# Kernel optimization log

Measured on AMD Instinct MI355X. Metric: run time of the kernel, lower is better.

## Reference

```python
import jax, jax.numpy as jnp
import numpy as np

OUT = 7  # out_size


def setup_inputs() -> dict:
    key = jax.random.key(0)
    kx, k1, k2, k3, k4 = jax.random.split(key, 5)
    B, C, H, W, Q = 4, 256, 128, 128, 100
    x = jax.random.normal(kx, (B, C, H, W), dtype=jnp.float32)
    # valid boxes: start in [0, W/2), extent in [8, W/2) -> always in-bounds, nonempty
    x1 = jax.random.randint(k1, (B, Q), 0, W // 2)
    y1 = jax.random.randint(k2, (B, Q), 0, H // 2)
    x2 = x1 + jax.random.randint(k3, (B, Q), 8, W // 2)
    y2 = y1 + jax.random.randint(k4, (B, Q), 8, H // 2)
    bidx = jnp.broadcast_to(jnp.arange(B, dtype=jnp.int32)[:, None], (B, Q))
    rois = jnp.stack([bidx, x1, y1, x2, y2], axis=-1).astype(jnp.int32)
    return {"x": x, "rois": rois}


def _bin_edges(start, length, nbins):
    # adaptive_avg_pool2d bin boundaries for bin k over a region of given length:
    #   lo_k = floor(k*L/n), hi_k = ceil((k+1)*L/n)
    # start, length: [B,Q] int; returns (starts, ends) each [B,Q,nbins]
    k = jnp.arange(nbins)
    lo = start[..., None] + (k * length[..., None]) // nbins
    hi = start[..., None] - ((-(k + 1) * length[..., None]) // nbins)  # ceil div
    return lo, hi


def reference(x, rois):
    # x: [B,C,H,W] float, rois: [B,Q,5] int (batch_idx, x1, y1, x2, y2)
    B, C, H, W = x.shape
    Q = rois.shape[1]
    oh = ow = OUT
    # Summed-area table S[b, y, x, c] = sum of x over rows < y, cols < x.
    xc = jnp.moveaxis(x, 1, -1)                       # [B,H,W,C]
    S = jnp.cumsum(jnp.cumsum(xc, axis=1), axis=2)
    S = jnp.pad(S, ((0, 0), (1, 0), (1, 0), (0, 0)))  # [B,H+1,W+1,C]

    x1, y1, x2, y2 = rois[..., 1], rois[..., 2], rois[..., 3], rois[..., 4]
    ys, ye = _bin_edges(y1, y2 - y1, oh)              # [B,Q,oh]
    xs, xe = _bin_edges(x1, x2 - x1, ow)              # [B,Q,ow]

    b = jnp.arange(B)[:, None, None, None]            # [B,1,1,1]
    Ys, Ye = ys[:, :, :, None], ye[:, :, :, None]     # [B,Q,oh,1]
    Xs, Xe = xs[:, :, None, :], xe[:, :, None, :]     # [B,Q,1,ow]

    # rectangle sums per bin via SAT corner differences -> [B,Q,oh,ow,C]
    sums = S[b, Ye, Xe] - S[b, Ys, Xe] - S[b, Ye, Xs] + S[b, Ys, Xs]
    area = ((Ye - Ys) * (Xe - Xs)).astype(x.dtype)[..., None]
    out = sums / area                                  # bin averages

    out = jnp.moveaxis(out, -1, 2)                     # [B,Q,C,oh,ow]
    return out.reshape(B, Q * C, oh, ow)               # cat ROIs along channel dim
```

## Files before the change

kernel.cpp:

```cpp
#include <hip/hip_runtime.h>

#define B_ 4
#define C_ 256
#define H_ 128
#define W_ 128
#define Q_ 100
#define WP_ 132

__global__ __launch_bounds__(512, 4) void roipool_kernel(const float4* __restrict__ x4,
                                                         const int* __restrict__ rois,
                                                         float* __restrict__ out) {
    __shared__ __align__(16) float sat[H_ * WP_];
    __shared__ float4 ot4[16 * 33];
    __shared__ unsigned int ebl[Q_ * 7];

    const int c   = blockIdx.x & 255;
    const int b   = blockIdx.x >> 8;
    const int tid = threadIdx.x;

    const float4* src = x4 + (size_t)(b * C_ + c) * (H_ * W_ / 4);
    const int wv = tid >> 6, ln = tid & 63;
    const int xl = ln & 31;
    #pragma unroll
    for (int i = 0; i < 8; ++i) {
        const int r = wv * 16 + i * 2 + (ln >> 5);
        float4 v = src[wv * 512 + i * 64 + ln];
        float s = v.x + v.y + v.z + v.w;
        float run = s;
        #pragma unroll
        for (int d = 1; d < 32; d <<= 1) {
            float t = __shfl_up(run, d);
            if (xl >= d) run += t;
        }
        const float excl = run - s;
        float4 o;
        o.x = excl + v.x;
        o.y = o.x + v.y;
        o.z = o.y + v.z;
        o.w = o.z + v.w;
        ((float4*)(sat + r * WP_))[xl] = o;
    }

    const int* rbase = rois + (size_t)b * Q_ * 5;
    for (int t = tid; t < Q_ * 7; t += 512) {
        const int q = t / 7;
        const int k = t - q * 7;
        const int* rb = rbase + q * 5;
        const int x1 = rb[1], y1 = rb[2];
        const int Lx = rb[3] - x1, Ly = rb[4] - y1;
        const unsigned int ys = y1 + (k * Ly) / 7;
        const unsigned int ye = y1 + ((k + 1) * Ly + 6) / 7;
        const unsigned int xs = x1 + (k * Lx) / 7;
        const unsigned int xe = x1 + ((k + 1) * Lx + 6) / 7;
        ebl[t] = ys | (ye << 8) | (xs << 16) | (xe << 24);
    }
    __syncthreads();

    {
        float4* s4 = (float4*)sat;
        const int oct = tid >> 5;
        const int stp = tid & 31;
        float4 acc = make_float4(0.f, 0.f, 0.f, 0.f);
        #pragma unroll
        for (int j = 0; j < 8; ++j) {
            const int y = oct * 8 + j;
            float4 v = s4[y * 33 + stp];
            acc.x += v.x; acc.y += v.y; acc.z += v.z; acc.w += v.w;
            s4[y * 33 + stp] = acc;
        }
        ot4[oct * 33 + stp] = acc;
    }
    __syncthreads();

    if (tid < 32) {
        float4 run = make_float4(0.f, 0.f, 0.f, 0.f);
        #pragma unroll
        for (int k = 0; k < 16; ++k) {
            float4 v = ot4[k * 33 + tid];
            ot4[k * 33 + tid] = run;
            run.x += v.x; run.y += v.y; run.z += v.z; run.w += v.w;
        }
    }
    __syncthreads();

    {
        float4* s4 = (float4*)sat;
        #pragma unroll
        for (int j = 0; j < 8; ++j) {
            const int f = j * 512 + tid;
            const int y = f >> 5;
            const int oc = y >> 3;
            const int st = f & 31;
            if (oc > 0) {
                float4 off = ot4[oc * 33 + st];
                float4 v = s4[y * 33 + st];
                v.x += off.x; v.y += off.y; v.z += off.z; v.w += off.w;
                s4[y * 33 + st] = v;
            }
        }
    }
    __syncthreads();

    float* ob = out + (size_t)(b * Q_) * (C_ * 49) + (size_t)c * 49;
    for (int t = tid; t < Q_ * 49; t += 512) {
        const int q   = t / 49;
        const int bin = t - q * 49;
        const int oy  = bin / 7;
        const int ox  = bin - oy * 7;

        const unsigned int ey = ebl[q * 7 + oy];
        const unsigned int ex = ebl[q * 7 + ox];
        const int ys = ey & 255;
        const int ye = (ey >> 8) & 255;
        const int xs = (ex >> 16) & 255;
        const int xe = ex >> 24;

        const float s11 = sat[(ye - 1) * WP_ + (xe - 1)];
        const float s01 = (ys > 0) ? sat[(ys - 1) * WP_ + (xe - 1)] : 0.f;
        const float s10 = (xs > 0) ? sat[(ye - 1) * WP_ + (xs - 1)] : 0.f;
        const float s00 = (ys > 0 && xs > 0) ? sat[(ys - 1) * WP_ + (xs - 1)] : 0.f;

        const float inv = __builtin_amdgcn_rcpf((float)((ye - ys) * (xe - xs)));
        ob[(size_t)q * (C_ * 49) + bin] = (s11 - s01 - s10 + s00) * inv;
    }
}

extern "C" void kernel_launch(void* const* d_in, const int* in_sizes, int n_in,
                              void* d_out, int out_size, void* d_ws, size_t ws_size,
                              hipStream_t stream) {
    const float* x    = (const float*)d_in[0];
    const int*   rois = (const int*)d_in[1];
    float*       outp = (float*)d_out;

    roipool_kernel<<<B_ * C_, 512, 0, stream>>>((const float4*)x, rois, outp);
}
```

Before: 108.1 us.

## Reorder SAT build: column scan from registers, then DPP row scan with padding

The summed-area table build is restructured. Global loads now feed the column prefix directly in registers instead of first scanning rows and writing to LDS. The row scan is fused with the column-offset fixup pass and uses DPP row-shift instructions in place of shfl_up. The table gains a zero row and a zero column at offset 3, so the query loop can drop its boundary branches. Together these remove one LDS read/write pass, the shuffle overhead and a barrier, at the cost of relying on wave-specific DPP semantics that must span a 32-lane half correctly.

```diff
diff --git a/kernel.cpp b/kernel.cpp
--- a/kernel.cpp
+++ b/kernel.cpp
@@ -5,12 +5,28 @@
 #define H_ 128
 #define W_ 128
 #define Q_ 100
-#define WP_ 132
+#define WROW 132
+#define NROW 129
+
+__device__ __forceinline__ float dpp_scan32(float s) {
+    int t;
+    t = __builtin_amdgcn_update_dpp(0, __float_as_int(s), 0x111, 0xf, 0xf, true);
+    s += __int_as_float(t);
+    t = __builtin_amdgcn_update_dpp(0, __float_as_int(s), 0x112, 0xf, 0xf, true);
+    s += __int_as_float(t);
+    t = __builtin_amdgcn_update_dpp(0, __float_as_int(s), 0x114, 0xf, 0xf, true);
+    s += __int_as_float(t);
+    t = __builtin_amdgcn_update_dpp(0, __float_as_int(s), 0x118, 0xf, 0xf, true);
+    s += __int_as_float(t);
+    t = __builtin_amdgcn_update_dpp(0, __float_as_int(s), 0x142, 0xa, 0xf, true);
+    s += __int_as_float(t);
+    return s;
+}
 
 __global__ __launch_bounds__(512, 4) void roipool_kernel(const float4* __restrict__ x4,
                                                          const int* __restrict__ rois,
                                                          float* __restrict__ out) {
-    __shared__ __align__(16) float sat[H_ * WP_];
+    __shared__ __align__(16) float sat[NROW * WROW];
     __shared__ float4 ot4[16 * 33];
     __shared__ unsigned int ebl[Q_ * 7];
 
@@ -18,30 +34,10 @@
     const int b   = blockIdx.x >> 8;
     const int tid = threadIdx.x;
 
-    const float4* src = x4 + (size_t)(b * C_ + c) * (H_ * W_ / 4);
-    const int wv = tid >> 6, ln = tid & 63;
-    const int xl = ln & 31;
-    #pragma unroll
-    for (int i = 0; i < 8; ++i) {
-        const int r = wv * 16 + i * 2 + (ln >> 5);
-        float4 v = src[wv * 512 + i * 64 + ln];
-        float s = v.x + v.y + v.z + v.w;
-        float run = s;
-        #pragma unroll
-        for (int d = 1; d < 32; d <<= 1) {
-            float t = __shfl_up(run, d);
-            if (xl >= d) run += t;
-        }
-        const float excl = run - s;
-        float4 o;
-        o.x = excl + v.x;
-        o.y = o.x + v.y;
-        o.z = o.y + v.z;
-        o.w = o.z + v.w;
-        ((float4*)(sat + r * WP_))[xl] = o;
-    }
+    if (tid < WROW) sat[tid] = 0.f;
+    else if (tid < WROW + 128) sat[(tid - WROW + 1) * WROW + 3] = 0.f;
 
-    const int* rbase = rois + (size_t)b * Q_ * 5;
+    const int* rbase = rois + b * Q_ * 5;
     for (int t = tid; t < Q_ * 7; t += 512) {
         const int q = t / 7;
         const int k = t - q * 7;
@@ -50,23 +46,24 @@
         const int Lx = rb[3] - x1, Ly = rb[4] - y1;
         const unsigned int ys = y1 + (k * Ly) / 7;
         const unsigned int ye = y1 + ((k + 1) * Ly + 6) / 7;
-        const unsigned int xs = x1 + (k * Lx) / 7;
-        const unsigned int xe = x1 + ((k + 1) * Lx + 6) / 7;
+        const unsigned int xs = x1 + (k * Lx) / 7 + 3;
+        const unsigned int xe = x1 + ((k + 1) * Lx + 6) / 7 + 3;
         ebl[t] = ys | (ye << 8) | (xs << 16) | (xe << 24);
     }
-    __syncthreads();
 
     {
-        float4* s4 = (float4*)sat;
         const int oct = tid >> 5;
         const int stp = tid & 31;
-        float4 acc = make_float4(0.f, 0.f, 0.f, 0.f);
+        const float4* src = x4 + (size_t)(b * C_ + c) * (H_ * W_ / 4);
+        float4 v[8];
+        #pragma unroll
+        for (int j = 0; j < 8; ++j)
+            v[j] = src[(oct * 8 + j) * 32 + stp];
+        float4 acc = v[0];
         #pragma unroll
         for (int j = 0; j < 8; ++j) {
-            const int y = oct * 8 + j;
-            float4 v = s4[y * 33 + stp];
-            acc.x += v.x; acc.y += v.y; acc.z += v.z; acc.w += v.w;
-            s4[y * 33 + stp] = acc;
+            if (j) { acc.x += v[j].x; acc.y += v[j].y; acc.z += v[j].z; acc.w += v[j].w; }
+            ((float4*)(sat + (oct * 8 + j + 1) * WROW + 4))[stp] = acc;
         }
         ot4[oct * 33 + stp] = acc;
     }
@@ -84,19 +81,24 @@
     __syncthreads();
 
     {
-        float4* s4 = (float4*)sat;
+        const int wv = tid >> 6, ln = tid & 63;
+        const int xl = ln & 31;
         #pragma unroll
-        for (int j = 0; j < 8; ++j) {
-            const int f = j * 512 + tid;
-            const int y = f >> 5;
-            const int oc = y >> 3;
-            const int st = f & 31;
-            if (oc > 0) {
-                float4 off = ot4[oc * 33 + st];
-                float4 v = s4[y * 33 + st];
-                v.x += off.x; v.y += off.y; v.z += off.z; v.w += off.w;
-                s4[y * 33 + st] = v;
-            }
+        for (int i = 0; i < 8; ++i) {
+            const int r = wv * 16 + i * 2 + (ln >> 5);
+            float4* p = (float4*)(sat + (r + 1) * WROW + 4);
+            float4 v = p[xl];
+            float4 off = ot4[(r >> 3) * 33 + xl];
+            v.x += off.x; v.y += off.y; v.z += off.z; v.w += off.w;
+            float s = v.x + v.y + v.z + v.w;
+            float run = dpp_scan32(s);
+            const float excl = run - s;
+            float4 o;
+            o.x = excl + v.x;
+            o.y = o.x + v.y;
+            o.z = o.y + v.z;
+            o.w = o.z + v.w;
+            p[xl] = o;
         }
     }
     __syncthreads();
@@ -110,18 +112,20 @@
 
         const unsigned int ey = ebl[q * 7 + oy];
         const unsigned int ex = ebl[q * 7 + ox];
-        const int ys = ey & 255;
-        const int ye = (ey >> 8) & 255;
-        const int xs = (ex >> 16) & 255;
-        const int xe = ex >> 24;
+        const int ys  = ey & 255;
+        const int ye  = (ey >> 8) & 255;
+        const int xs3 = (ex >> 16) & 255;
+        const int xe3 = ex >> 24;
 
-        const float s11 = sat[(ye - 1) * WP_ + (xe - 1)];
-        const float s01 = (ys > 0) ? sat[(ys - 1) * WP_ + (xe - 1)] : 0.f;
-        const float s10 = (xs > 0) ? sat[(ye - 1) * WP_ + (xs - 1)] : 0.f;
-        const float s00 = (ys > 0 && xs > 0) ? sat[(ys - 1) * WP_ + (xs - 1)] : 0.f;
+        const int ylo = ys * WROW;
+        const int yhi = ye * WROW;
+        const float s11 = sat[yhi + xe3];
+        const float s01 = sat[ylo + xe3];
+        const float s10 = sat[yhi + xs3];
+        const float s00 = sat[ylo + xs3];
 
-        const float inv = __builtin_amdgcn_rcpf((float)((ye - ys) * (xe - xs)));
-        ob[(size_t)q * (C_ * 49) + bin] = (s11 - s01 - s10 + s00) * inv;
+        const float inv = __builtin_amdgcn_rcpf((float)((ye - ys) * (xe3 - xs3)));
+        ob[(size_t)q * (C_ * 49) + bin] = ((s11 - s01) - (s10 - s00)) * inv;
     }
 }
 
```

After: 106.2 us. Within noise of the previous version (-1.7%).
